# Optimization experiments

Hardware: AMD Instinct MI355X
Metric: run time of the kernel (lower is better)

Reference implementation:

```python
import jax, jax.numpy as jnp
import numpy as np


def _conv1x1(x, W, b):
    # x: (n, c_in, h, w); W: (c_out, c_in); b: (c_out,)
    return jnp.einsum('nchw,oc->nohw', x, W) + b[None, :, None, None]


def setup_inputs() -> dict:
    key = jax.random.key(0)
    ks = jax.random.split(key, 9)
    n, C, h, w = 2, 256, 64, 64
    Ch = C // 2
    s_in = 0.02
    return {
        'feature': jax.random.normal(ks[0], (n, C, h, w), dtype=jnp.float32),
        'Wq': jax.random.normal(ks[1], (Ch, C), dtype=jnp.float32) * s_in,
        'bq': jax.random.normal(ks[2], (Ch,), dtype=jnp.float32) * s_in,
        'Wk': jax.random.normal(ks[3], (Ch, C), dtype=jnp.float32) * s_in,
        'bk': jax.random.normal(ks[4], (Ch,), dtype=jnp.float32) * s_in,
        'Wv': jax.random.normal(ks[5], (Ch, C), dtype=jnp.float32) * s_in,
        'bv': jax.random.normal(ks[6], (Ch,), dtype=jnp.float32) * s_in,
        'Wm': jax.random.normal(ks[7], (C, Ch), dtype=jnp.float32) * s_in,
        'bm': jax.random.normal(ks[8], (C,), dtype=jnp.float32) * s_in,
    }


def reference(feature, Wq, bq, Wk, bk, Wv, bv, Wm, bm):
    n, C, h, w = feature.shape
    Ch = C // 2
    N = n * h * w
    # 1x1 conv projections, then flatten batch+spatial into one sequence dim
    q = _conv1x1(feature, Wq, bq)  # (n, Ch, h, w)
    k = _conv1x1(feature, Wk, bk)
    v = _conv1x1(feature, Wv, bv)
    # NCHW -> NHWC -> (N, Ch), matching torch transpose(1,2).transpose(2,3).reshape
    q = jnp.transpose(q, (0, 2, 3, 1)).reshape(N, Ch)
    k = jnp.transpose(k, (0, 2, 3, 1)).reshape(N, Ch)
    v = jnp.transpose(v, (0, 2, 3, 1)).reshape(N, Ch)
    # scores = k @ q.T (note: torch code uses k as rows, q.T as cols)
    scores = k @ q.T  # (N, N)
    attn = jax.nn.softmax(scores, axis=-1)
    mask = attn @ v  # (N, Ch)
    mask = mask.reshape(n, h, w, Ch)
    # torch transpose chain (2,3)->(1,2)->(2,3): (n,h,w,Ch) -> (n,Ch,w,h)
    mask = jnp.transpose(mask, (0, 3, 2, 1))
    out = _conv1x1(mask, Wm, bm)  # (n, C, w, h); h==w so residual add is valid
    return out + feature
```

## Files before the change

### kernel.cpp

```cpp
#include <hip/hip_runtime.h>
#include <hip/hip_bf16.h>

#define LOG2E 1.44269504088896340736f

typedef __attribute__((ext_vector_type(8))) short short8;
typedef __attribute__((ext_vector_type(4))) float f32x4;
typedef __attribute__((ext_vector_type(16))) float f32x16;
typedef __attribute__((ext_vector_type(2))) unsigned int uint2v;
typedef __attribute__((ext_vector_type(4))) unsigned int uint4v;
typedef unsigned int u32;

__device__ __forceinline__ short f2bf(float f) {
    unsigned u = __builtin_bit_cast(unsigned, f);
    unsigned r = (u + 0x7FFFu + ((u >> 16) & 1u)) >> 16;
    return (short)r;
}

__device__ __forceinline__ float bf2f(short x) {
    unsigned u = ((unsigned)(unsigned short)x) << 16;
    return __builtin_bit_cast(float, u);
}

__device__ __forceinline__ unsigned cvt_pk_bf16(float lo, float hi) {
    unsigned r;
    asm volatile("v_cvt_pk_bf16_f32 %0, %1, %2" : "=v"(r) : "v"(lo), "v"(hi));
    return r;
}

__device__ __forceinline__ float fexp2(float x) {
    float r;
    asm("v_exp_f32 %0, %1" : "=v"(r) : "v"(x));
    return r;
}

__global__ __launch_bounds__(64) void wprep_kernel(
    const float* __restrict__ Wq, const float* __restrict__ bq,
    const float* __restrict__ Wk, const float* __restrict__ bk,
    const float* __restrict__ Wv, const float* __restrict__ bv,
    const float* __restrict__ Wm,
    short* __restrict__ Wb, float* __restrict__ bqkv, short* __restrict__ Wmb)
{
    const int b = blockIdx.x;
    const int t = threadIdx.x;
    if (b < 384) {
        const int mat = b >> 7, row = b & 127;
        const float* src = (mat == 0 ? Wq : mat == 1 ? Wk : Wv) + (size_t)row * 256;
        const float sc = (mat == 1) ? LOG2E : 1.f;
        float4 v = *(const float4*)(src + t * 4);
        uint2v pk;
        pk.x = cvt_pk_bf16(v.x * sc, v.y * sc);
        pk.y = cvt_pk_bf16(v.z * sc, v.w * sc);
        *(uint2v*)(Wb + (size_t)b * 256 + t * 4) = pk;
    } else if (b == 384) {
        for (int e = t; e < 384; e += 64) {
            const int mat = e >> 7;
            const float* bsrc = (mat == 0 ? bq : mat == 1 ? bk : bv);
            bqkv[e] = bsrc[e & 127] * (mat == 1 ? LOG2E : 1.f);
        }
    } else {
        const int row = b - 385;
        float2 v = *(const float2*)(Wm + (size_t)row * 128 + t * 2);
        *(u32*)(Wmb + (size_t)row * 128 + t * 2) = cvt_pk_bf16(v.x, v.y);
    }
}

__global__ __launch_bounds__(256) void proj_kernel(
    const float* __restrict__ feat, const short* __restrict__ Wb,
    const float* __restrict__ bqkv,
    short* __restrict__ Qg, short* __restrict__ Kg, short* __restrict__ Vg)
{
    __shared__ __align__(16) short Xs[16 * 256];
    __shared__ __align__(16) short VTs[128 * 16];
    const int t = threadIdx.x;
    const int blk = blockIdx.x;
    const int ib = blk * 16;
    const int n = ib >> 12;
    const int hw0 = ib & 4095;

    {
        const int r0 = (t & 3) * 4;
        const int c0 = (t >> 2) * 4;
        const float* fp = feat + (size_t)n * 1048576 + (size_t)c0 * 4096 + hw0 + r0;
        f32x4 v0 = *(const f32x4*)(fp);
        f32x4 v1 = *(const f32x4*)(fp + 4096);
        f32x4 v2 = *(const f32x4*)(fp + 8192);
        f32x4 v3 = *(const f32x4*)(fp + 12288);
        #pragma unroll
        for (int k = 0; k < 4; ++k) {
            uint2v pk;
            pk.x = cvt_pk_bf16(v0[k], v1[k]);
            pk.y = cvt_pk_bf16(v2[k], v3[k]);
            const int r = r0 + k;
            const int sw = (r & 7) << 2;
            *(uint2v*)(&Xs[r * 256 + (((c0 >> 3) ^ sw) * 8) + (c0 & 7)]) = pk;
        }
    }
    __syncthreads();

    const int lane = t & 63;
    const int w = __builtin_amdgcn_readfirstlane(t >> 6);
    const int l15 = lane & 15;
    const int g = lane >> 4;
    const int o0w = w * 96;

    f32x4 acc[6];
    #pragma unroll
    for (int osub = 0; osub < 6; ++osub)
        acc[osub] = *(const f32x4*)(bqkv + o0w + osub * 16 + 4 * g);

    const short* wbase = Wb + (size_t)(o0w + l15) * 256 + g * 8;
    const int xsw = (l15 & 7) << 2;
    #pragma unroll
    for (int kc = 0; kc < 8; ++kc) {
        short8 xf = *(const short8*)(&Xs[l15 * 256 + (((kc * 4 + g) ^ xsw) * 8)]);
        #pragma unroll
        for (int osub = 0; osub < 6; ++osub) {
            short8 wf = *(const short8*)(wbase + (size_t)osub * 16 * 256 + kc * 32);
            acc[osub] = __builtin_amdgcn_mfma_f32_16x16x32_bf16(wf, xf, acc[osub], 0, 0, 0);
        }
    }

    #pragma unroll
    for (int osub = 0; osub < 6; ++osub) {
        const int o0 = o0w + osub * 16;
        const int mat = o0 >> 7;
        if (mat < 2) {
            const int ch0 = (o0 & 127) + 4 * g;
            const int kc = ch0 >> 4;
            const int hh = (ch0 >> 3) & 1;
            const int e0 = ch0 & 7;
            const int j = ib + l15;
            short* dst = (mat == 0 ? Qg : Kg)
                + (size_t)(j >> 5) * 4096 + kc * 512 + ((j & 31) + 32 * hh) * 8 + e0;
            uint2v pk;
            pk.x = cvt_pk_bf16(acc[osub][0], acc[osub][1]);
            pk.y = cvt_pk_bf16(acc[osub][2], acc[osub][3]);
            *(uint2v*)dst = pk;
        } else {
            const int col = (o0 & 127) + 4 * g;
            #pragma unroll
            for (int reg = 0; reg < 4; ++reg)
                VTs[(col + reg) * 16 + l15] = f2bf(acc[osub][reg]);
        }
    }
    __syncthreads();

    {
        const int o = t >> 1, ih = (t & 1) * 8;
        short8 vv = *(const short8*)(&VTs[o * 16 + ih]);
        const int jt = ib >> 5;
        const int nn = (ib >> 4) & 1;
        short* vb = Vg + (size_t)jt * 4096 + (o >> 5) * 1024 + nn * 512
                      + (o & 31) * 8 + (ih >> 1);
        uint4v q = __builtin_bit_cast(uint4v, vv);
        uint2v lo; lo.x = q.x; lo.y = q.y;
        uint2v hi; hi.x = q.z; hi.y = q.w;
        *(uint2v*)(vb) = lo;
        *(uint2v*)(vb + 256) = hi;
    }
}

__global__ __launch_bounds__(256, 2) void attn_kernel(
    const short* __restrict__ Qg, const short* __restrict__ Kg,
    const short* __restrict__ Vg,
    short* __restrict__ Opart, float* __restrict__ Ssb)
{
    __shared__ __align__(16) char smem[65536];

    const int tid = threadIdx.x;
    const int lane = tid & 63;
    const int w = __builtin_amdgcn_readfirstlane(tid >> 6);
    const int l31 = lane & 31;
    const int h = lane >> 5;
    const int blk = blockIdx.x;
    const int ibX = blk >> 3;
    const int jq  = blk & 7;
    const int iw  = ibX * 128 + w * 32;
    const int j0  = jq * 1024;

    short8 kf[8];
    {
        const short* kp = Kg + (size_t)(iw >> 5) * 4096 + lane * 8;
        #pragma unroll
        for (int kc = 0; kc < 8; ++kc) kf[kc] = *(const short8*)(kp + kc * 512);
    }

    f32x16 O[4];
    #pragma unroll
    for (int dc = 0; dc < 4; ++dc)
        #pragma unroll
        for (int e = 0; e < 16; ++e) O[dc][e] = 0.f;
    float s = 0.f;

    const short* srcQ = Qg + (size_t)(j0 >> 5) * 4096 + w * 512 + lane * 8;
    const short* srcV = Vg + (size_t)(j0 >> 5) * 4096 + w * 512 + lane * 8;

    auto stage = [&](int quarter) {
        char* base = smem + quarter * 16384;
        __builtin_amdgcn_global_load_lds(
            (const __attribute__((address_space(1))) u32*)(const void*)srcQ,
            (__attribute__((address_space(3))) u32*)(void*)(base + w * 1024), 16, 0, 0);
        __builtin_amdgcn_global_load_lds(
            (const __attribute__((address_space(1))) u32*)(const void*)(srcQ + 2048),
            (__attribute__((address_space(3))) u32*)(void*)(base + (4 + w) * 1024), 16, 0, 0);
        __builtin_amdgcn_global_load_lds(
            (const __attribute__((address_space(1))) u32*)(const void*)srcV,
            (__attribute__((address_space(3))) u32*)(void*)(base + 8192 + w * 1024), 16, 0, 0);
        __builtin_amdgcn_global_load_lds(
            (const __attribute__((address_space(1))) u32*)(const void*)(srcV + 2048),
            (__attribute__((address_space(3))) u32*)(void*)(base + 8192 + (4 + w) * 1024), 16, 0, 0);
        srcQ += 4096;
        srcV += 4096;
    };

    auto compute32 = [&](const char* base) {
        const char* Qt = base;
        const char* Vt = base + 8192;

        f32x16 sva, svb;
        #pragma unroll
        for (int e = 0; e < 16; ++e) { sva[e] = -16.f; svb[e] = 0.f; }

        __builtin_amdgcn_s_setprio(1);
        #pragma unroll
        for (int kc = 0; kc < 4; ++kc) {
            short8 qa0 = *(const short8*)(Qt + (2 * kc) * 1024 + lane * 16);
            short8 qa1 = *(const short8*)(Qt + (2 * kc + 1) * 1024 + lane * 16);
            sva = __builtin_amdgcn_mfma_f32_32x32x16_bf16(qa0, kf[2 * kc], sva, 0, 0, 0);
            svb = __builtin_amdgcn_mfma_f32_32x32x16_bf16(qa1, kf[2 * kc + 1], svb, 0, 0, 0);
        }
        __builtin_amdgcn_s_setprio(0);

        float p[16];
        #pragma unroll
        for (int r = 0; r < 16; ++r) p[r] = fexp2(sva[r] + svb[r]);
        float q0 = (p[0] + p[1]) + (p[2] + p[3]);
        float q1 = (p[4] + p[5]) + (p[6] + p[7]);
        float q2 = (p[8] + p[9]) + (p[10] + p[11]);
        float q3 = (p[12] + p[13]) + (p[14] + p[15]);
        s += (q0 + q1) + (q2 + q3);

        short8 pf0, pf1;
        {
            uint4v a, b;
            a.x = cvt_pk_bf16(p[0], p[1]);  a.y = cvt_pk_bf16(p[2], p[3]);
            a.z = cvt_pk_bf16(p[4], p[5]);  a.w = cvt_pk_bf16(p[6], p[7]);
            b.x = cvt_pk_bf16(p[8], p[9]);  b.y = cvt_pk_bf16(p[10], p[11]);
            b.z = cvt_pk_bf16(p[12], p[13]); b.w = cvt_pk_bf16(p[14], p[15]);
            pf0 = __builtin_bit_cast(short8, a);
            pf1 = __builtin_bit_cast(short8, b);
        }

        __builtin_amdgcn_s_setprio(1);
        #pragma unroll
        for (int dc = 0; dc < 4; ++dc) {
            short8 va0 = *(const short8*)(Vt + dc * 2048 + lane * 16);
            short8 va1 = *(const short8*)(Vt + dc * 2048 + 1024 + lane * 16);
            O[dc] = __builtin_amdgcn_mfma_f32_32x32x16_bf16(va0, pf0, O[dc], 0, 0, 0);
            O[dc] = __builtin_amdgcn_mfma_f32_32x32x16_bf16(va1, pf1, O[dc], 0, 0, 0);
        }
        __builtin_amdgcn_s_setprio(0);
    };

    stage(0);
    stage(1);
    stage(2);
    for (int tt = 0; tt < 30; ++tt) {
        asm volatile("s_waitcnt vmcnt(8)" ::: "memory");
        __builtin_amdgcn_s_barrier();
        __builtin_amdgcn_sched_barrier(0);
        if (tt < 29) stage((tt + 3) & 3);
        compute32(smem + (tt & 3) * 16384);
    }
    asm volatile("s_waitcnt vmcnt(4)" ::: "memory");
    __builtin_amdgcn_s_barrier();
    __builtin_amdgcn_sched_barrier(0);
    compute32(smem + (30 & 3) * 16384);
    asm volatile("s_waitcnt vmcnt(0)" ::: "memory");
    __builtin_amdgcn_s_barrier();
    __builtin_amdgcn_sched_barrier(0);
    compute32(smem + (31 & 3) * 16384);

    {
        const int i = iw + l31;
        short* op = Opart + ((size_t)i * 8 + jq) * 128;
        #pragma unroll
        for (int dc = 0; dc < 4; ++dc) {
            #pragma unroll
            for (int q4 = 0; q4 < 4; ++q4) {
                uint2v pk;
                pk.x = cvt_pk_bf16(O[dc][4 * q4 + 0], O[dc][4 * q4 + 1]);
                pk.y = cvt_pk_bf16(O[dc][4 * q4 + 2], O[dc][4 * q4 + 3]);
                *(uint2v*)(op + dc * 32 + q4 * 8 + 4 * h) = pk;
            }
        }
        Ssb[((size_t)i * 8 + jq) * 2 + h] = s;
    }
}

__global__ __launch_bounds__(256, 4) void epi_kernel(
    const short* __restrict__ Opart, const float* __restrict__ Ssb,
    const short* __restrict__ Wmb, const float* __restrict__ bm,
    const float* __restrict__ feat, float* __restrict__ out)
{
    __shared__ __align__(16) short Ms[16 * 128];
    const int t = threadIdx.x;
    const int blk = blockIdx.x;
    const int yt = blk & 3;
    const int x = (blk >> 2) & 63;
    const int n = blk >> 8;
    const int y0 = yt * 16;

    {
        const int r = t >> 4, c = t & 15;
        const int i = n * 4096 + (y0 + r) * 64 + x;
        float acc8[8] = {0.f, 0.f, 0.f, 0.f, 0.f, 0.f, 0.f, 0.f};
        #pragma unroll
        for (int q = 0; q < 8; ++q) {
            short8 o = *(const short8*)(Opart + ((size_t)i * 8 + q) * 128 + c * 8);
            #pragma unroll
            for (int e = 0; e < 8; ++e) acc8[e] += bf2f(o[e]);
        }
        float tp = Ssb[(size_t)i * 16 + c];
        tp += __shfl_xor(tp, 1);
        tp += __shfl_xor(tp, 2);
        tp += __shfl_xor(tp, 4);
        tp += __shfl_xor(tp, 8);
        const float inv = 1.f / tp;
        uint4v pk;
        pk.x = cvt_pk_bf16(acc8[0] * inv, acc8[1] * inv);
        pk.y = cvt_pk_bf16(acc8[2] * inv, acc8[3] * inv);
        pk.z = cvt_pk_bf16(acc8[4] * inv, acc8[5] * inv);
        pk.w = cvt_pk_bf16(acc8[6] * inv, acc8[7] * inv);
        *(short8*)(&Ms[r * 128 + ((c ^ ((r & 7) << 1)) * 8)]) =
            __builtin_bit_cast(short8, pk);
    }
    __syncthreads();

    const int lane = t & 63;
    const int w = __builtin_amdgcn_readfirstlane(t >> 6);
    const int l15 = lane & 15;
    const int g = lane >> 4;
    const int c0 = w * 64;

    short8 bf[4];
    const int msw = (l15 & 7) << 1;
    #pragma unroll
    for (int dcq = 0; dcq < 4; ++dcq)
        bf[dcq] = *(const short8*)(&Ms[l15 * 128 + (((dcq * 4 + g) ^ msw) * 8)]);

    f32x4 acc[4];
    #pragma unroll
    for (int ct = 0; ct < 4; ++ct)
        acc[ct] = *(const f32x4*)(bm + c0 + ct * 16 + 4 * g);

    const short* wbase = Wmb + (size_t)(c0 + l15) * 128 + g * 8;
    #pragma unroll
    for (int dcq = 0; dcq < 4; ++dcq) {
        #pragma unroll
        for (int ct = 0; ct < 4; ++ct) {
            short8 wf = *(const short8*)(wbase + (size_t)ct * 16 * 128 + dcq * 32);
            acc[ct] = __builtin_amdgcn_mfma_f32_16x16x32_bf16(wf, bf[dcq], acc[ct], 0, 0, 0);
        }
    }

    #pragma unroll
    for (int ct = 0; ct < 4; ++ct) {
        #pragma unroll
        for (int reg = 0; reg < 4; ++reg) {
            const int c = c0 + ct * 16 + 4 * g + reg;
            const size_t oidx = (((size_t)(n * 256 + c) * 64 + x) * 64) + y0 + l15;
            out[oidx] = acc[ct][reg] + feat[oidx];
        }
    }
}

extern "C" void kernel_launch(void* const* d_in, const int* in_sizes, int n_in,
                              void* d_out, int out_size, void* d_ws, size_t ws_size,
                              hipStream_t stream) {
    const float* feat = (const float*)d_in[0];
    const float* Wq = (const float*)d_in[1];
    const float* bq = (const float*)d_in[2];
    const float* Wk = (const float*)d_in[3];
    const float* bk = (const float*)d_in[4];
    const float* Wv = (const float*)d_in[5];
    const float* bv = (const float*)d_in[6];
    const float* Wm = (const float*)d_in[7];
    const float* bm = (const float*)d_in[8];
    float* out = (float*)d_out;

    short* Qg = (short*)d_ws;
    short* Kg = Qg + 8192 * 128;
    short* Vg = Kg + 8192 * 128;
    short* Opart = Vg + 8192 * 128;
    float* Ssb = (float*)(Opart + (size_t)8 * 8192 * 128);
    float* bqkv = Ssb + (size_t)8192 * 16;
    short* Wb = (short*)(bqkv + 384);
    short* Wmb = Wb + 384 * 256;

    hipLaunchKernelGGL(wprep_kernel, dim3(641), dim3(64), 0, stream,
                       Wq, bq, Wk, bk, Wv, bv, Wm, Wb, bqkv, Wmb);
    hipLaunchKernelGGL(proj_kernel, dim3(512), dim3(256), 0, stream,
                       feat, Wb, bqkv, Qg, Kg, Vg);
    hipLaunchKernelGGL(attn_kernel, dim3(512), dim3(256), 0, stream,
                       Qg, Kg, Vg, Opart, Ssb);
    hipLaunchKernelGGL(epi_kernel, dim3(512), dim3(256), 0, stream,
                       Opart, Ssb, Wmb, bm, feat, out);
}
```

Measured before the change: 74.34 us.

## Give each wave two 32-row query tiles and split keys into 16 chunks

Each wave now owns 64 rows, held as two 32-row K fragment sets, so every Q and V fragment loaded from LDS feeds two MFMA chains. The key range per block halves (16 splits of 512 instead of 8 of 1024), and the epilogue reduces 16 partial outputs and sums. This raises MFMA reuse of LDS data per wave but doubles accumulator registers and the partial-output traffic the epilogue must read. It also drops the two-accumulator split of the score reduction in favour of a single chain per tile.

```diff
diff --git a/kernel.cpp b/kernel.cpp
--- a/kernel.cpp
+++ b/kernel.cpp
@@ -173,24 +173,27 @@
     const int l31 = lane & 31;
     const int h = lane >> 5;
     const int blk = blockIdx.x;
-    const int ibX = blk >> 3;
-    const int jq  = blk & 7;
-    const int iw  = ibX * 128 + w * 32;
-    const int j0  = jq * 1024;
-
-    short8 kf[8];
+    const int ibX = blk >> 4;
+    const int jq  = blk & 15;
+    const int iw  = ibX * 256 + w * 64;
+    const int j0  = jq * 512;
+
+    short8 kfA[8], kfB[8];
     {
         const short* kp = Kg + (size_t)(iw >> 5) * 4096 + lane * 8;
         #pragma unroll
-        for (int kc = 0; kc < 8; ++kc) kf[kc] = *(const short8*)(kp + kc * 512);
-    }
-
-    f32x16 O[4];
+        for (int kc = 0; kc < 8; ++kc) {
+            kfA[kc] = *(const short8*)(kp + kc * 512);
+            kfB[kc] = *(const short8*)(kp + 4096 + kc * 512);
+        }
+    }
+
+    f32x16 OA[4], OB[4];
     #pragma unroll
     for (int dc = 0; dc < 4; ++dc)
         #pragma unroll
-        for (int e = 0; e < 16; ++e) O[dc][e] = 0.f;
-    float s = 0.f;
+        for (int e = 0; e < 16; ++e) { OA[dc][e] = 0.f; OB[dc][e] = 0.f; }
+    float sA = 0.f, sB = 0.f;
 
     const short* srcQ = Qg + (size_t)(j0 >> 5) * 4096 + w * 512 + lane * 8;
     const short* srcV = Vg + (size_t)(j0 >> 5) * 4096 + w * 512 + lane * 8;
@@ -217,38 +220,49 @@
         const char* Qt = base;
         const char* Vt = base + 8192;
 
-        f32x16 sva, svb;
-        #pragma unroll
-        for (int e = 0; e < 16; ++e) { sva[e] = -16.f; svb[e] = 0.f; }
+        f32x16 svA, svB;
+        #pragma unroll
+        for (int e = 0; e < 16; ++e) { svA[e] = -16.f; svB[e] = -16.f; }
 
         __builtin_amdgcn_s_setprio(1);
         #pragma unroll
-        for (int kc = 0; kc < 4; ++kc) {
-            short8 qa0 = *(const short8*)(Qt + (2 * kc) * 1024 + lane * 16);
-            short8 qa1 = *(const short8*)(Qt + (2 * kc + 1) * 1024 + lane * 16);
-            sva = __builtin_amdgcn_mfma_f32_32x32x16_bf16(qa0, kf[2 * kc], sva, 0, 0, 0);
-            svb = __builtin_amdgcn_mfma_f32_32x32x16_bf16(qa1, kf[2 * kc + 1], svb, 0, 0, 0);
+        for (int kc = 0; kc < 8; ++kc) {
+            short8 qa = *(const short8*)(Qt + kc * 1024 + lane * 16);
+            svA = __builtin_amdgcn_mfma_f32_32x32x16_bf16(qa, kfA[kc], svA, 0, 0, 0);
+            svB = __builtin_amdgcn_mfma_f32_32x32x16_bf16(qa, kfB[kc], svB, 0, 0, 0);
         }
         __builtin_amdgcn_s_setprio(0);
 
-        float p[16];
-        #pragma unroll
-        for (int r = 0; r < 16; ++r) p[r] = fexp2(sva[r] + svb[r]);
-        float q0 = (p[0] + p[1]) + (p[2] + p[3]);
-        float q1 = (p[4] + p[5]) + (p[6] + p[7]);
-        float q2 = (p[8] + p[9]) + (p[10] + p[11]);
-        float q3 = (p[12] + p[13]) + (p[14] + p[15]);
-        s += (q0 + q1) + (q2 + q3);
-
-        short8 pf0, pf1;
+        short8 pfA0, pfA1, pfB0, pfB1;
         {
+            float p[16];
+            #pragma unroll
+            for (int r = 0; r < 16; ++r) p[r] = fexp2(svA[r]);
+            float q0 = (p[0]+p[1])+(p[2]+p[3]), q1 = (p[4]+p[5])+(p[6]+p[7]);
+            float q2 = (p[8]+p[9])+(p[10]+p[11]), q3 = (p[12]+p[13])+(p[14]+p[15]);
+            sA += (q0 + q1) + (q2 + q3);
             uint4v a, b;
             a.x = cvt_pk_bf16(p[0], p[1]);  a.y = cvt_pk_bf16(p[2], p[3]);
             a.z = cvt_pk_bf16(p[4], p[5]);  a.w = cvt_pk_bf16(p[6], p[7]);
             b.x = cvt_pk_bf16(p[8], p[9]);  b.y = cvt_pk_bf16(p[10], p[11]);
             b.z = cvt_pk_bf16(p[12], p[13]); b.w = cvt_pk_bf16(p[14], p[15]);
-            pf0 = __builtin_bit_cast(short8, a);
-            pf1 = __builtin_bit_cast(short8, b);
+            pfA0 = __builtin_bit_cast(short8, a);
+            pfA1 = __builtin_bit_cast(short8, b);
+        }
+        {
+            float p[16];
+            #pragma unroll
+            for (int r = 0; r < 16; ++r) p[r] = fexp2(svB[r]);
+            float q0 = (p[0]+p[1])+(p[2]+p[3]), q1 = (p[4]+p[5])+(p[6]+p[7]);
+            float q2 = (p[8]+p[9])+(p[10]+p[11]), q3 = (p[12]+p[13])+(p[14]+p[15]);
+            sB += (q0 + q1) + (q2 + q3);
+            uint4v a, b;
+            a.x = cvt_pk_bf16(p[0], p[1]);  a.y = cvt_pk_bf16(p[2], p[3]);
+            a.z = cvt_pk_bf16(p[4], p[5]);  a.w = cvt_pk_bf16(p[6], p[7]);
+            b.x = cvt_pk_bf16(p[8], p[9]);  b.y = cvt_pk_bf16(p[10], p[11]);
+            b.z = cvt_pk_bf16(p[12], p[13]); b.w = cvt_pk_bf16(p[14], p[15]);
+            pfB0 = __builtin_bit_cast(short8, a);
+            pfB1 = __builtin_bit_cast(short8, b);
         }
 
         __builtin_amdgcn_s_setprio(1);
@@ -256,8 +270,10 @@
         for (int dc = 0; dc < 4; ++dc) {
             short8 va0 = *(const short8*)(Vt + dc * 2048 + lane * 16);
             short8 va1 = *(const short8*)(Vt + dc * 2048 + 1024 + lane * 16);
-            O[dc] = __builtin_amdgcn_mfma_f32_32x32x16_bf16(va0, pf0, O[dc], 0, 0, 0);
-            O[dc] = __builtin_amdgcn_mfma_f32_32x32x16_bf16(va1, pf1, O[dc], 0, 0, 0);
+            OA[dc] = __builtin_amdgcn_mfma_f32_32x32x16_bf16(va0, pfA0, OA[dc], 0, 0, 0);
+            OA[dc] = __builtin_amdgcn_mfma_f32_32x32x16_bf16(va1, pfA1, OA[dc], 0, 0, 0);
+            OB[dc] = __builtin_amdgcn_mfma_f32_32x32x16_bf16(va0, pfB0, OB[dc], 0, 0, 0);
+            OB[dc] = __builtin_amdgcn_mfma_f32_32x32x16_bf16(va1, pfB1, OB[dc], 0, 0, 0);
         }
         __builtin_amdgcn_s_setprio(0);
     };
@@ -265,36 +281,38 @@
     stage(0);
     stage(1);
     stage(2);
-    for (int tt = 0; tt < 30; ++tt) {
+    for (int tt = 0; tt < 14; ++tt) {
         asm volatile("s_waitcnt vmcnt(8)" ::: "memory");
         __builtin_amdgcn_s_barrier();
         __builtin_amdgcn_sched_barrier(0);
-        if (tt < 29) stage((tt + 3) & 3);
+        if (tt < 13) stage((tt + 3) & 3);
         compute32(smem + (tt & 3) * 16384);
     }
     asm volatile("s_waitcnt vmcnt(4)" ::: "memory");
     __builtin_amdgcn_s_barrier();
     __builtin_amdgcn_sched_barrier(0);
-    compute32(smem + (30 & 3) * 16384);
+    compute32(smem + (14 & 3) * 16384);
     asm volatile("s_waitcnt vmcnt(0)" ::: "memory");
     __builtin_amdgcn_s_barrier();
     __builtin_amdgcn_sched_barrier(0);
-    compute32(smem + (31 & 3) * 16384);
-
-    {
-        const int i = iw + l31;
-        short* op = Opart + ((size_t)i * 8 + jq) * 128;
+    compute32(smem + (15 & 3) * 16384);
+
+    #pragma unroll
+    for (int iset = 0; iset < 2; ++iset) {
+        const int i = iw + iset * 32 + l31;
+        const f32x16* Op = iset == 0 ? OA : OB;
+        short* op = Opart + ((size_t)i * 16 + jq) * 128;
         #pragma unroll
         for (int dc = 0; dc < 4; ++dc) {
             #pragma unroll
             for (int q4 = 0; q4 < 4; ++q4) {
                 uint2v pk;
-                pk.x = cvt_pk_bf16(O[dc][4 * q4 + 0], O[dc][4 * q4 + 1]);
-                pk.y = cvt_pk_bf16(O[dc][4 * q4 + 2], O[dc][4 * q4 + 3]);
+                pk.x = cvt_pk_bf16(Op[dc][4 * q4 + 0], Op[dc][4 * q4 + 1]);
+                pk.y = cvt_pk_bf16(Op[dc][4 * q4 + 2], Op[dc][4 * q4 + 3]);
                 *(uint2v*)(op + dc * 32 + q4 * 8 + 4 * h) = pk;
             }
         }
-        Ssb[((size_t)i * 8 + jq) * 2 + h] = s;
+        Ssb[(i * 32) + jq * 2 + h] = (iset == 0 ? sA : sB);
     }
 }
 
@@ -316,12 +334,13 @@
         const int i = n * 4096 + (y0 + r) * 64 + x;
         float acc8[8] = {0.f, 0.f, 0.f, 0.f, 0.f, 0.f, 0.f, 0.f};
         #pragma unroll
-        for (int q = 0; q < 8; ++q) {
-            short8 o = *(const short8*)(Opart + ((size_t)i * 8 + q) * 128 + c * 8);
+        for (int q = 0; q < 16; ++q) {
+            short8 o = *(const short8*)(Opart + ((size_t)i * 16 + q) * 128 + c * 8);
             #pragma unroll
             for (int e = 0; e < 8; ++e) acc8[e] += bf2f(o[e]);
         }
-        float tp = Ssb[(size_t)i * 16 + c];
+        float2 s2 = *(const float2*)(Ssb + (size_t)i * 32 + c * 2);
+        float tp = s2.x + s2.y;
         tp += __shfl_xor(tp, 1);
         tp += __shfl_xor(tp, 2);
         tp += __shfl_xor(tp, 4);
@@ -393,8 +412,8 @@
     short* Kg = Qg + 8192 * 128;
     short* Vg = Kg + 8192 * 128;
     short* Opart = Vg + 8192 * 128;
-    float* Ssb = (float*)(Opart + (size_t)8 * 8192 * 128);
-    float* bqkv = Ssb + (size_t)8192 * 16;
+    float* Ssb = (float*)(Opart + (size_t)16 * 8192 * 128);
+    float* bqkv = Ssb + (size_t)8192 * 32;
     short* Wb = (short*)(bqkv + 384);
     short* Wmb = Wb + 384 * 256;
 
```

New measurement: 86.71 us. 1.17x slower.
